# Optimization experiments

Measured on AMD Instinct MI355X. Metric: run time of the kernel, lower is better.

## Reference

```python
import jax, jax.numpy as jnp
import numpy as np

D_MODEL = 2048
N_HEADS = 16
N_KV_HEADS = 4
DH = D_MODEL // N_HEADS          # 128
GROUPS = N_HEADS // N_KV_HEADS   # 4
ROPE_BASE = 10000.0
B, T = 2, 2048


def _rope_tables(positions):
    # positions: [T] int -> cos,sin [T, DH//2]
    inv = 1.0 / (ROPE_BASE ** (jnp.arange(0, DH, 2, dtype=jnp.float32) / DH))
    ang = positions.astype(jnp.float32)[:, None] * inv[None, :]
    return jnp.cos(ang), jnp.sin(ang)


def _apply_rope(x, cos, sin):
    # x: [B,H,T,DH]; cos/sin: [1,1,T,DH//2]; interleaved even/odd rotation
    even, odd = x[..., ::2], x[..., 1::2]
    xe = even * cos - odd * sin
    xo = even * sin + odd * cos
    return jnp.stack([xe, xo], axis=-1).reshape(x.shape)


def setup_inputs() -> dict:
    key = jax.random.key(0)
    k1, k2, k3 = jax.random.split(key, 3)
    qkv_dim = D_MODEL + 2 * N_KV_HEADS * DH
    x = jax.random.normal(k1, (B, T, D_MODEL), dtype=jnp.float32)
    Wqkv = jax.random.normal(k2, (D_MODEL, qkv_dim), dtype=jnp.float32) / np.sqrt(D_MODEL).astype(np.float32)
    Wo = jax.random.normal(k3, (N_HEADS * DH, D_MODEL), dtype=jnp.float32) / np.sqrt(N_HEADS * DH).astype(np.float32)
    return {"x": x, "Wqkv": Wqkv, "Wo": Wo, "start_pos": 0}


def reference(x, Wqkv, Wo, start_pos):
    Bx, Tx, _ = x.shape
    qkv = x @ Wqkv  # [B,T,D + 2*HKV*DH]
    q, k, v = jnp.split(qkv, [N_HEADS * DH, N_HEADS * DH + N_KV_HEADS * DH], axis=-1)
    q = q.reshape(Bx, Tx, N_HEADS, DH).transpose(0, 2, 1, 3)      # [B,H,T,DH]
    k = k.reshape(Bx, Tx, N_KV_HEADS, DH).transpose(0, 2, 1, 3)   # [B,HKV,T,DH]
    v = v.reshape(Bx, Tx, N_KV_HEADS, DH).transpose(0, 2, 1, 3)

    pos = start_pos + jnp.arange(Tx)
    cos, sin = _rope_tables(pos)
    cos = cos[None, None]; sin = sin[None, None]
    q = _apply_rope(q, cos, sin)
    k = _apply_rope(k, cos, sin)

    # GQA: repeat_interleave kv heads
    k = jnp.repeat(k, GROUPS, axis=1)  # [B,H,T,DH]
    v = jnp.repeat(v, GROUPS, axis=1)

    scale = 1.0 / np.sqrt(DH).astype(np.float32)
    att = jnp.einsum('bhqd,bhkd->bhqk', q, k) * scale
    causal = jnp.triu(jnp.ones((Tx, Tx), dtype=bool), 1)
    att = jnp.where(causal[None, None], jnp.float32(-jnp.inf), att)
    att = jax.nn.softmax(att, axis=-1)
    y = jnp.einsum('bhqk,bhkd->bhqd', att, v)
    y = y.transpose(0, 2, 1, 3).reshape(Bx, Tx, N_HEADS * DH)
    return y @ Wo
```

## Files before the change

kernel.cpp:

```cpp
#include <hip/hip_runtime.h>
#include <math.h>

#define D_MODEL 2048
#define N_HEADS 16
#define N_KV    4
#define DH      128
#define QKV_DIM 3072
#define TT      2048
#define BB      2
#define ROWS    (BB*TT)

#define KS_STRIDE 136
#define VS_STRIDE 72
#define PS_STRIDE 72

typedef unsigned short u16;
typedef short short8 __attribute__((ext_vector_type(8)));
typedef short short4v __attribute__((ext_vector_type(4)));
typedef float float4v __attribute__((ext_vector_type(4)));

__device__ inline float b2f(u16 h) {
    union { unsigned u; float f; } v; v.u = ((unsigned)h) << 16; return v.f;
}
__device__ inline u16 f2b(float f) {
    union { float f; unsigned u; } v; v.f = f;
    unsigned r = v.u + 0x7FFF + ((v.u >> 16) & 1);
    return (u16)(r >> 16);
}

__device__ inline void async16(const void* g, void* l) {
    __builtin_amdgcn_global_load_lds(
        (const __attribute__((address_space(1))) void*)g,
        (__attribute__((address_space(3))) void*)l, 16, 0, 0);
}

__device__ inline float rope_rot(float v, int row, int col, int sp0) {
    float partner = __shfl_xor(v, 1, 64);
    int t = row & (TT - 1);
    int ii = (col & 127) >> 1;
    float ang = (float)(sp0 + t) * expf(-0.14391156816f * (float)ii);
    float c = cosf(ang), s = sinf(ang);
    return (col & 1) ? (partner * s + v * c)
                     : (v * c - partner * s);
}

__global__ void convert_f2b(const float* __restrict__ src, u16* __restrict__ dst) {
    int i = blockIdx.x * 256 + threadIdx.x;
    float4v a = *(const float4v*)(src + (size_t)i * 4);
    short4v p;
    p[0] = (short)f2b(a[0]); p[1] = (short)f2b(a[1]);
    p[2] = (short)f2b(a[2]); p[3] = (short)f2b(a[3]);
    *(short4v*)(dst + (size_t)i * 4) = p;
}

__global__ void transpose_f2b(const float* __restrict__ src, u16* __restrict__ dst,
                              int R, int C, int col0) {
    __shared__ __align__(16) u16 tile[32][33];
    int bc = blockIdx.x * 32, br = blockIdx.y * 32;
    int tx = threadIdx.x & 31, ty = threadIdx.x >> 5;
    for (int i = ty; i < 32; i += 8)
        tile[i][tx] = f2b(src[(size_t)(br + i) * C + col0 + bc + tx]);
    __syncthreads();
    for (int i = ty; i < 32; i += 8)
        dst[(size_t)(bc + i) * R + br + tx] = tile[tx][i];
}

template<bool F32OUT, bool ROPE>
__global__ __launch_bounds__(256) void gemm_bt_async(
    const u16* __restrict__ A, const u16* __restrict__ Bt1, const u16* __restrict__ Bt2,
    int nsplit, void* __restrict__ Cv, int M, int N, int K, const int* __restrict__ sp) {
    __shared__ __align__(16) u16 As[128 * 32];
    __shared__ __align__(16) u16 Bs[128 * 32];
    const int tid = threadIdx.x;
    const int wave = tid >> 6, lane = tid & 63;
    const int quad = lane >> 4, l16 = lane & 15;
    const int bm = blockIdx.y * 128, bn = blockIdx.x * 128;
    const int wm = (wave >> 1) * 64, wn = (wave & 1) * 64;
    const int srow = wave * 32 + (lane >> 2);
    const int scol = (lane & 3) * 8;
    const u16* Bt = (bn < nsplit) ? (Bt1 + (size_t)bn * K)
                                  : (Bt2 + (size_t)(bn - nsplit) * K);

    float4v acc[4][4] = {};

    for (int k0 = 0; k0 < K; k0 += 32) {
        async16(A + (size_t)(bm + srow) * K + k0 + scol, (char*)As + wave * 2048);
        async16(A + (size_t)(bm + srow + 16) * K + k0 + scol, (char*)As + wave * 2048 + 1024);
        async16(Bt + (size_t)srow * K + k0 + scol, (char*)Bs + wave * 2048);
        async16(Bt + (size_t)(srow + 16) * K + k0 + scol, (char*)Bs + wave * 2048 + 1024);
        __syncthreads();
        short8 af[4], bf[4];
#pragma unroll
        for (int i = 0; i < 4; i++)
            af[i] = *(const short8*)(As + (wm + i * 16 + l16) * 32 + quad * 8);
#pragma unroll
        for (int j = 0; j < 4; j++)
            bf[j] = *(const short8*)(Bs + (wn + j * 16 + l16) * 32 + quad * 8);
#pragma unroll
        for (int i = 0; i < 4; i++)
#pragma unroll
            for (int j = 0; j < 4; j++)
                acc[i][j] = __builtin_amdgcn_mfma_f32_16x16x32_bf16(af[i], bf[j], acc[i][j], 0, 0, 0);
        __syncthreads();
    }
    const int sp0 = ROPE ? *sp : 0;
#pragma unroll
    for (int i = 0; i < 4; i++) {
        int row0 = bm + wm + i * 16 + quad * 4;
#pragma unroll
        for (int j = 0; j < 4; j++) {
            int col = bn + wn + j * 16 + l16;
            bool do_rope = ROPE && (col < 2560);
#pragma unroll
            for (int r = 0; r < 4; r++) {
                float v = acc[i][j][r];
                if (do_rope) v = rope_rot(v, row0 + r, col, sp0);
                if (F32OUT) ((float*)Cv)[(size_t)(row0 + r) * N + col] = v;
                else        ((u16*)Cv)[(size_t)(row0 + r) * N + col] = f2b(v);
            }
        }
    }
}

__global__ __launch_bounds__(512) void attn_kernel(
    const u16* __restrict__ qkv, u16* __restrict__ y) {
    __shared__ __align__(16) u16 Ks[64 * KS_STRIDE];
    __shared__ __align__(16) u16 Vs[128 * VS_STRIDE];
    __shared__ __align__(16) u16 Ps[8][16 * PS_STRIDE];

    const int tid = threadIdx.x;
    const int wave = tid >> 6, lane = tid & 63;
    const int quad = lane >> 4, l16 = lane & 15;
    const int bx = blockIdx.x;
    const int xg = bx & 7;
    const int b = xg >> 2, hk = xg & 3;
    const int jj = bx >> 3;
    const int h = hk * 4 + (jj & 3);
    const int qq = jj >> 2;
    const int qt = (qq & 1) ? (15 - (qq >> 1)) : (qq >> 1);
    const int qcol = h * 128;
    const int kcol = 2048 + hk * 128;
    const int vcol = 2560 + hk * 128;
    const float scale = 0.08838834764831845f;

    const int wq0 = qt * 128 + wave * 16;
    const u16* qrow = qkv + (size_t)(b * TT + wq0 + l16) * QKV_DIM + qcol;
    short8 qf[4];
#pragma unroll
    for (int d = 0; d < 4; d++)
        qf[d] = *(const short8*)(qrow + d * 32 + quad * 8);

    float4v Oacc[9] = {};
    const short8 ONES = {(short)0x3F80, (short)0x3F80, (short)0x3F80, (short)0x3F80,
                         (short)0x3F80, (short)0x3F80, (short)0x3F80, (short)0x3F80};

    const int ktmax = 2 * qt + 1;
    const int krow = ((tid) >> 4) & 31;
    const int kcv = lane & 15;
    short8 kreg[2], vreg[2];
    {
        const u16* base = qkv + (size_t)(b * TT) * QKV_DIM;
#pragma unroll
        for (int s = 0; s < 2; s++) {
            int row = s * 32 + krow;
            kreg[s] = *(const short8*)(base + (size_t)row * QKV_DIM + kcol + kcv * 8);
            vreg[s] = *(const short8*)(base + (size_t)lane * QKV_DIM + vcol + (wave * 2 + s) * 8);
        }
    }

    for (int kt = 0; kt <= ktmax; kt++) {
        __syncthreads();
#pragma unroll
        for (int s = 0; s < 2; s++) {
            int row = s * 32 + krow;
            *(short8*)(Ks + row * KS_STRIDE + kcv * 8) = kreg[s];
            int dgi = wave * 2 + s;
#pragma unroll
            for (int j8 = 0; j8 < 8; j8++)
                Vs[(dgi * 8 + j8) * VS_STRIDE + lane] = (u16)vreg[s][j8];
        }
        __syncthreads();
        if (kt < ktmax) {
            const u16* base = qkv + (size_t)(b * TT + (kt + 1) * 64) * QKV_DIM;
#pragma unroll
            for (int s = 0; s < 2; s++) {
                int row = s * 32 + krow;
                kreg[s] = *(const short8*)(base + (size_t)row * QKV_DIM + kcol + kcv * 8);
                vreg[s] = *(const short8*)(base + (size_t)lane * QKV_DIM + vcol + (wave * 2 + s) * 8);
            }
        }

        float4v S[4] = {};
#pragma unroll
        for (int d = 0; d < 4; d++) {
#pragma unroll
            for (int j = 0; j < 4; j++) {
                short8 bk = *(const short8*)(Ks + (j * 16 + l16) * KS_STRIDE + d * 32 + quad * 8);
                S[j] = __builtin_amdgcn_mfma_f32_16x16x32_bf16(qf[d], bk, S[j], 0, 0, 0);
            }
        }
        const int qbase = wq0 + quad * 4;
        const int kvb = kt * 64 + l16;
        const bool diag = (kt * 64 + 63 > wq0);
#pragma unroll
        for (int j = 0; j < 4; j++)
#pragma unroll
            for (int r = 0; r < 4; r++) {
                bool masked = diag && (kvb + j * 16 > qbase + r);
                float p = masked ? 0.f : __expf(S[j][r] * scale);
                Ps[wave][(quad * 4 + r) * PS_STRIDE + j * 16 + l16] = f2b(p);
            }
        __asm__ volatile("s_waitcnt lgkmcnt(0)" ::: "memory");
#pragma unroll
        for (int ks = 0; ks < 2; ks++) {
            short8 ap = *(const short8*)(Ps[wave] + l16 * PS_STRIDE + ks * 32 + quad * 8);
#pragma unroll
            for (int dt = 0; dt < 8; dt++) {
                short8 bv = *(const short8*)(Vs + (dt * 16 + l16) * VS_STRIDE + ks * 32 + quad * 8);
                Oacc[dt] = __builtin_amdgcn_mfma_f32_16x16x32_bf16(ap, bv, Oacc[dt], 0, 0, 0);
            }
            Oacc[8] = __builtin_amdgcn_mfma_f32_16x16x32_bf16(ap, ONES, Oacc[8], 0, 0, 0);
        }
    }
#pragma unroll
    for (int dt = 0; dt < 8; dt++)
#pragma unroll
        for (int r = 0; r < 4; r++) {
            float v = Oacc[dt][r] / Oacc[8][r];
            y[(size_t)(b * TT + wq0 + quad * 4 + r) * D_MODEL
              + h * 128 + dt * 16 + l16] = f2b(v);
        }
}

extern "C" void kernel_launch(void* const* d_in, const int* in_sizes, int n_in,
                              void* d_out, int out_size, void* d_ws, size_t ws_size,
                              hipStream_t stream) {
    const float* x    = (const float*)d_in[0];
    const float* Wqkv = (const float*)d_in[1];
    const float* Wo   = (const float*)d_in[2];
    const int*   sp   = (const int*)d_in[3];

    char* ws = (char*)d_ws;
    char* dob = (char*)d_out;
    u16*   xb     = (u16*)ws;
    u16*   Y      = (u16*)ws;
    u16*   WqkvTA = (u16*)(ws + 16777216);
    u16*   WoT    = (u16*)(ws + 16777216);
    u16*   QKV    = (u16*)d_out;
    u16*   WqkvTB = (u16*)(dob + 25165824);
    float* out    = (float*)d_out;

    convert_f2b<<<ROWS * D_MODEL / 4 / 256, 256, 0, stream>>>(x, xb);
    transpose_f2b<<<dim3(64, 64), 256, 0, stream>>>(Wqkv, WqkvTA, D_MODEL, QKV_DIM, 0);
    transpose_f2b<<<dim3(32, 64), 256, 0, stream>>>(Wqkv, WqkvTB, D_MODEL, QKV_DIM, 2048);
    gemm_bt_async<false, true><<<dim3(QKV_DIM / 128, ROWS / 128), 256, 0, stream>>>(
        xb, WqkvTA, WqkvTB, 2048, QKV, ROWS, QKV_DIM, D_MODEL, sp);
    transpose_f2b<<<dim3(64, 64), 256, 0, stream>>>(Wo, WoT, D_MODEL, D_MODEL, 0);
    attn_kernel<<<512, 512, 0, stream>>>(QKV, Y);
    gemm_bt_async<true, false><<<dim3(D_MODEL / 128, ROWS / 128), 256, 0, stream>>>(
        Y, WoT, WoT, D_MODEL, out, ROWS, D_MODEL, D_MODEL, sp);
}
```

Measured before the change: 367.2 us.

## Double-buffer K tiles via async LDS loads and cheapen RoPE epilogue

In the attention kernel, K tiles are now fetched straight into a double-buffered LDS array with global_load_lds, replacing the register staging and explicit LDS stores. The row padding of the K buffer is dropped so the async layout fits. The aim is to overlap the next tile's fetch with compute and cut register and VALU traffic, at the risk of LDS bank conflicts on the unpadded 256-byte rows. In the GEMM epilogue, the RoPE inverse frequency is hoisted per column, and precise expf/cosf/sinf are replaced with fast intrinsics, which trades some accuracy for fewer transcendental instructions.

```diff
diff --git a/kernel.cpp b/kernel.cpp
--- a/kernel.cpp
+++ b/kernel.cpp
@@ -10,7 +10,6 @@
 #define BB      2
 #define ROWS    (BB*TT)
 
-#define KS_STRIDE 136
 #define VS_STRIDE 72
 #define PS_STRIDE 72
 
@@ -32,16 +31,6 @@
     __builtin_amdgcn_global_load_lds(
         (const __attribute__((address_space(1))) void*)g,
         (__attribute__((address_space(3))) void*)l, 16, 0, 0);
-}
-
-__device__ inline float rope_rot(float v, int row, int col, int sp0) {
-    float partner = __shfl_xor(v, 1, 64);
-    int t = row & (TT - 1);
-    int ii = (col & 127) >> 1;
-    float ang = (float)(sp0 + t) * expf(-0.14391156816f * (float)ii);
-    float c = cosf(ang), s = sinf(ang);
-    return (col & 1) ? (partner * s + v * c)
-                     : (v * c - partner * s);
 }
 
 __global__ void convert_f2b(const float* __restrict__ src, u16* __restrict__ dst) {
@@ -105,16 +94,24 @@
     }
     const int sp0 = ROPE ? *sp : 0;
 #pragma unroll
-    for (int i = 0; i < 4; i++) {
-        int row0 = bm + wm + i * 16 + quad * 4;
-#pragma unroll
-        for (int j = 0; j < 4; j++) {
-            int col = bn + wn + j * 16 + l16;
-            bool do_rope = ROPE && (col < 2560);
+    for (int j = 0; j < 4; j++) {
+        int col = bn + wn + j * 16 + l16;
+        bool do_rope = ROPE && (col < 2560);
+        float inv = 0.f;
+        if (do_rope) inv = __expf(-0.14391156816f * (float)((col & 127) >> 1));
+#pragma unroll
+        for (int i = 0; i < 4; i++) {
+            int row0 = bm + wm + i * 16 + quad * 4;
 #pragma unroll
             for (int r = 0; r < 4; r++) {
                 float v = acc[i][j][r];
-                if (do_rope) v = rope_rot(v, row0 + r, col, sp0);
+                if (do_rope) {
+                    float partner = __shfl_xor(v, 1, 64);
+                    float ang = (float)(sp0 + ((row0 + r) & (TT - 1))) * inv;
+                    float c = __cosf(ang), s = __sinf(ang);
+                    v = (col & 1) ? (partner * s + v * c)
+                                  : (v * c - partner * s);
+                }
                 if (F32OUT) ((float*)Cv)[(size_t)(row0 + r) * N + col] = v;
                 else        ((u16*)Cv)[(size_t)(row0 + r) * N + col] = f2b(v);
             }
@@ -124,7 +121,7 @@
 
 __global__ __launch_bounds__(512) void attn_kernel(
     const u16* __restrict__ qkv, u16* __restrict__ y) {
-    __shared__ __align__(16) u16 Ks[64 * KS_STRIDE];
+    __shared__ __align__(16) u16 Ks[2][64 * 128];
     __shared__ __align__(16) u16 Vs[128 * VS_STRIDE];
     __shared__ __align__(16) u16 Ps[8][16 * PS_STRIDE];
 
@@ -155,25 +152,20 @@
                          (short)0x3F80, (short)0x3F80, (short)0x3F80, (short)0x3F80};
 
     const int ktmax = 2 * qt + 1;
-    const int krow = ((tid) >> 4) & 31;
-    const int kcv = lane & 15;
-    short8 kreg[2], vreg[2];
-    {
-        const u16* base = qkv + (size_t)(b * TT) * QKV_DIM;
+
+    const size_t kgoff = (size_t)(wave * 8 + (lane >> 4)) * QKV_DIM + (lane & 15) * 8;
+    async16(qkv + (size_t)(b * TT) * QKV_DIM + kcol + kgoff, (char*)Ks[0] + wave * 2048);
+    async16(qkv + (size_t)(b * TT + 4) * QKV_DIM + kcol + kgoff, (char*)Ks[0] + wave * 2048 + 1024);
+    short8 vreg[2];
+#pragma unroll
+    for (int s = 0; s < 2; s++)
+        vreg[s] = *(const short8*)(qkv + (size_t)(b * TT + lane) * QKV_DIM + vcol + (wave * 2 + s) * 8);
+
+    for (int kt = 0; kt <= ktmax; kt++) {
+        const u16* Kcur = Ks[kt & 1];
+        __syncthreads();
 #pragma unroll
         for (int s = 0; s < 2; s++) {
-            int row = s * 32 + krow;
-            kreg[s] = *(const short8*)(base + (size_t)row * QKV_DIM + kcol + kcv * 8);
-            vreg[s] = *(const short8*)(base + (size_t)lane * QKV_DIM + vcol + (wave * 2 + s) * 8);
-        }
-    }
-
-    for (int kt = 0; kt <= ktmax; kt++) {
-        __syncthreads();
-#pragma unroll
-        for (int s = 0; s < 2; s++) {
-            int row = s * 32 + krow;
-            *(short8*)(Ks + row * KS_STRIDE + kcv * 8) = kreg[s];
             int dgi = wave * 2 + s;
 #pragma unroll
             for (int j8 = 0; j8 < 8; j8++)
@@ -181,13 +173,13 @@
         }
         __syncthreads();
         if (kt < ktmax) {
-            const u16* base = qkv + (size_t)(b * TT + (kt + 1) * 64) * QKV_DIM;
-#pragma unroll
-            for (int s = 0; s < 2; s++) {
-                int row = s * 32 + krow;
-                kreg[s] = *(const short8*)(base + (size_t)row * QKV_DIM + kcol + kcv * 8);
-                vreg[s] = *(const short8*)(base + (size_t)lane * QKV_DIM + vcol + (wave * 2 + s) * 8);
-            }
+            const u16* kb = qkv + (size_t)(b * TT + (kt + 1) * 64) * QKV_DIM;
+            async16(kb + kcol + kgoff, (char*)Ks[(kt + 1) & 1] + wave * 2048);
+            async16(kb + (size_t)4 * QKV_DIM + kcol + kgoff,
+                    (char*)Ks[(kt + 1) & 1] + wave * 2048 + 1024);
+#pragma unroll
+            for (int s = 0; s < 2; s++)
+                vreg[s] = *(const short8*)(kb + (size_t)lane * QKV_DIM + vcol + (wave * 2 + s) * 8);
         }
 
         float4v S[4] = {};
@@ -195,7 +187,7 @@
         for (int d = 0; d < 4; d++) {
 #pragma unroll
             for (int j = 0; j < 4; j++) {
-                short8 bk = *(const short8*)(Ks + (j * 16 + l16) * KS_STRIDE + d * 32 + quad * 8);
+                short8 bk = *(const short8*)(Kcur + (j * 16 + l16) * 128 + d * 32 + quad * 8);
                 S[j] = __builtin_amdgcn_mfma_f32_16x16x32_bf16(qf[d], bk, S[j], 0, 0, 0);
             }
         }
```

New measurement: 416.5 us. 1.13x slower.
